# Optimization experiments

Hardware: AMD Instinct MI355X
Metric: run time of the kernel (lower is better)

Reference implementation:

```python
import jax, jax.numpy as jnp
import numpy as np

EMA_A = 0.4      # exponential moving average decay used in Hash_ExpMovAverage
WIN = 9          # window_size
LN_EPS = 1e-3    # keras LayerNormalization default epsilon


def setup_inputs() -> dict:
    key = jax.random.key(0)
    ks = jax.random.split(key, 8)
    B, N, D, H = 8, 4096, 256, 8
    w = lambda k, shape: jax.random.normal(k, shape, jnp.float32) * 0.05
    return {
        "x": jax.random.normal(ks[0], (B, N, D), jnp.float32),
        "head_kernel": w(ks[1], (D, H, D)),
        "head_bias": w(ks[2], (H, D)),
        "down_kernel": w(ks[3], (H, D, D)),
        "down_bias": w(ks[4], (D,)),
        "value_kernel": w(ks[5], (D, D)),
        "value_bias": w(ks[6], (D,)),
        "ln_gamma": jnp.ones((D,), jnp.float32),
        "ln_beta": jnp.zeros((D,), jnp.float32),
    }


def reference(x, head_kernel, head_bias, down_kernel, down_bias,
              value_kernel, value_bias, ln_gamma, ln_beta):
    B, N, D = x.shape
    half = (WIN - 1) // 2

    # Up_Projection: [B,N,D] -> [B,N,H,D], relu
    q = jax.nn.relu(jnp.einsum('bnd,dhe->bnhe', x, head_kernel) + head_bias)

    # ---- Neighborhoods_Arrangement ----
    # Neighborhood_SimHash: sign codes from relu activations, summed over heads
    codes = 2.0 * jnp.minimum(jnp.ceil(q), 1.0) - 1.0        # [B,N,H,D]
    lsh = jnp.sum(codes, axis=-2)                            # [B,N,D]
    # Hash_ExpMovAverage: sort descending along D, add positional encoding, EMA dot
    pos = jnp.argsort(-lsh, axis=-1)                         # descending order
    lsh_sorted = jnp.take_along_axis(lsh, pos, axis=-1)
    pf = pos.astype(jnp.float32)
    freq = 10.0 ** (-(pf / jnp.float32(D)))                  # 1 / 10**powers
    pe = jnp.sin(freq) * (pf % 2) + jnp.cos(freq) * (1.0 - pf % 2)
    vals = lsh_sorted + pe / EMA_A
    c = EMA_A * (1.0 - EMA_A) ** jnp.arange(D, dtype=jnp.float32)
    simv = jnp.einsum('bnd,d->bn', vals, c)                  # [B,N]
    order = jnp.argsort(simv, axis=-1)                       # ascending
    q = jnp.take_along_axis(q, order[:, :, None, None], axis=1)  # reorder tokens

    # Down_Projection: [B,N,H,D] -> [B,N,D], relu
    q = jax.nn.relu(jnp.einsum('bnhd,hde->bne', q, down_kernel) + down_bias)

    # (matches tile-first / extract_patches / tile-last concat in the original)
    starts = jnp.clip(jnp.arange(N) - half, 0, N - WIN)      # [N]
    widx = starts[:, None] + jnp.arange(WIN)[None, :]
    keyw = q[:, widx]

    scale = jnp.sqrt(jnp.float32(D))
    scores = jax.nn.softmax(jnp.einsum('bnd,bnwd->bnw', q, keyw) / scale, axis=-1)
    value = jax.nn.relu(jnp.einsum('bnwd,de->bnwe', keyw, value_kernel) + value_bias)
    attn_out = jnp.einsum('bnwd,bnw->bnd', value, scores)

    # Residual with ORIGINAL (un-permuted) inputs + LayerNorm (keras default eps)
    y = attn_out + x
    mu = jnp.mean(y, axis=-1, keepdims=True)
    var = jnp.var(y, axis=-1, keepdims=True)
    return (y - mu) / jnp.sqrt(var + LN_EPS) * ln_gamma + ln_beta
```

## Files before the change

### kernel.cpp

```cpp
#include <hip/hip_runtime.h>

constexpr int Bc = 8, Nc = 4096;

using short8 = __attribute__((ext_vector_type(8))) short;
using f32x4  = __attribute__((ext_vector_type(4))) float;

static __device__ __forceinline__ unsigned short f2bf(float f) {
    unsigned u = __float_as_uint(f);
    u += 0x7fffu + ((u >> 16) & 1u);
    return (unsigned short)(u >> 16);
}
static __device__ __forceinline__ int swz(int r, int k) {
    return (r << 9) + ((k << 1) ^ ((r & 7) << 4));
}

#define GBIN_CAP 320
#define GUARD    0.012f

__global__ __launch_bounds__(256)
void k0_wdt(const float* __restrict__ Wd, unsigned short* __restrict__ WdT)
{
    __shared__ float tile[64][65];
    const int h  = blockIdx.x >> 4;
    const int t  = blockIdx.x & 15;
    const int kb = (t >> 2) * 64, eb = (t & 3) * 64;
    const int tid = threadIdx.x;
    {
        const int krow = tid >> 2, ec = (tid & 3) * 16;
        const float* src = Wd + h * 65536 + (kb + krow) * 256 + eb + ec;
        #pragma unroll
        for (int i = 0; i < 4; ++i) {
            float4 v = *reinterpret_cast<const float4*>(src + i * 4);
            tile[krow][ec + i * 4 + 0] = v.x;
            tile[krow][ec + i * 4 + 1] = v.y;
            tile[krow][ec + i * 4 + 2] = v.z;
            tile[krow][ec + i * 4 + 3] = v.w;
        }
    }
    __syncthreads();
    {
        const int erow = tid >> 2, dc = (tid & 3) * 16;
        unsigned short o[16];
        #pragma unroll
        for (int i = 0; i < 16; ++i) o[i] = f2bf(tile[dc + i][erow]);
        unsigned short* dst = WdT + h * 65536 + (eb + erow) * 256 + kb + dc;
        *reinterpret_cast<short8*>(dst)     = *reinterpret_cast<short8*>(&o[0]);
        *reinterpret_cast<short8*>(dst + 8) = *reinterpret_cast<short8*>(&o[8]);
    }
}

__global__ __launch_bounds__(256)
void k0_wht(const float* __restrict__ Wh, unsigned short* __restrict__ WhH,
            float* __restrict__ WhT)
{
    __shared__ float tile[64][65];
    const int h  = blockIdx.x >> 4;
    const int t  = blockIdx.x & 15;
    const int kb = (t >> 2) * 64, eb = (t & 3) * 64;
    const int tid = threadIdx.x;
    {
        const int krow = tid >> 2, ec = (tid & 3) * 16;
        const float* src = Wh + (kb + krow) * 2048 + h * 256 + eb + ec;
        #pragma unroll
        for (int i = 0; i < 4; ++i) {
            float4 v = *reinterpret_cast<const float4*>(src + i * 4);
            tile[krow][ec + i * 4 + 0] = v.x;
            tile[krow][ec + i * 4 + 1] = v.y;
            tile[krow][ec + i * 4 + 2] = v.z;
            tile[krow][ec + i * 4 + 3] = v.w;
        }
    }
    __syncthreads();
    {
        const int erow = tid >> 2, dc = (tid & 3) * 16;
        unsigned short o[16];
        float of[16];
        #pragma unroll
        for (int i = 0; i < 16; ++i) {
            of[i] = tile[dc + i][erow];
            o[i] = f2bf(of[i]);
        }
        const long base = (long)h * 65536 + (eb + erow) * 256 + kb + dc;
        *reinterpret_cast<short8*>(WhH + base)     = *reinterpret_cast<short8*>(&o[0]);
        *reinterpret_cast<short8*>(WhH + base + 8) = *reinterpret_cast<short8*>(&o[8]);
        #pragma unroll
        for (int i = 0; i < 16; i += 4)
            *reinterpret_cast<float4*>(WhT + base + i) = *reinterpret_cast<const float4*>(&of[i]);
    }
}

__global__ __launch_bounds__(256)
void k0_wvt(const float* __restrict__ Wv, unsigned short* __restrict__ WvT)
{
    __shared__ float tile[64][65];
    const int t  = blockIdx.x;
    const int kb = (t >> 2) * 64, eb = (t & 3) * 64;
    const int tid = threadIdx.x;
    {
        const int krow = tid >> 2, ec = (tid & 3) * 16;
        const float* src = Wv + (kb + krow) * 256 + eb + ec;
        #pragma unroll
        for (int i = 0; i < 4; ++i) {
            float4 v = *reinterpret_cast<const float4*>(src + i * 4);
            tile[krow][ec + i * 4 + 0] = v.x;
            tile[krow][ec + i * 4 + 1] = v.y;
            tile[krow][ec + i * 4 + 2] = v.z;
            tile[krow][ec + i * 4 + 3] = v.w;
        }
    }
    __syncthreads();
    {
        const int erow = tid >> 2, dc = (tid & 3) * 16;
        unsigned short o[16];
        #pragma unroll
        for (int i = 0; i < 16; ++i) o[i] = f2bf(tile[dc + i][erow]);
        unsigned short* dst = WvT + (eb + erow) * 256 + kb + dc;
        *reinterpret_cast<short8*>(dst)     = *reinterpret_cast<short8*>(&o[0]);
        *reinterpret_cast<short8*>(dst + 8) = *reinterpret_cast<short8*>(&o[8]);
    }
}

__global__ __launch_bounds__(256, 3)
void k1a_head(const float* __restrict__ x, const float* __restrict__ bh,
              const unsigned short* __restrict__ WhH,
              unsigned short* __restrict__ q, int* __restrict__ gcnt, int* __restrict__ gls)
{
    __shared__ __align__(16) char SM[16384];

    const int tid = threadIdx.x;
    const long rowbase = (long)blockIdx.x * 32;
    const int h = blockIdx.y;
    const int wavei = tid >> 6, lane = tid & 63;
    const int mrow = lane & 15, kgrp = lane >> 4;
    const int ebase = wavei * 64 + mrow;
    const int kfo = kgrp * 8;
    const unsigned short* whh = WhH + ((long)h << 16);

    short8 hB[4][4];
    #pragma unroll
    for (int i = 0; i < 4; ++i)
        #pragma unroll
        for (int nf = 0; nf < 4; ++nf)
            hB[i][nf] = *reinterpret_cast<const short8*>(
                &whh[(ebase + nf * 16) * 256 + i * 32 + kfo]);

    {
        const int r = tid >> 3, kc = (tid & 7) * 32;
        const float* src = x + (rowbase + r) * 256 + kc;
        unsigned short oh[32];
        #pragma unroll
        for (int i = 0; i < 32; i += 4) {
            float4 v = *reinterpret_cast<const float4*>(src + i);
            oh[i + 0] = f2bf(v.x); oh[i + 1] = f2bf(v.y);
            oh[i + 2] = f2bf(v.z); oh[i + 3] = f2bf(v.w);
        }
        #pragma unroll
        for (int i = 0; i < 32; i += 8)
            *reinterpret_cast<short8*>(SM + swz(r, kc + i)) =
                *reinterpret_cast<short8*>(&oh[i]);
    }
    __syncthreads();

    f32x4 hacc[2][4];
    #pragma unroll
    for (int mt = 0; mt < 2; ++mt)
        #pragma unroll
        for (int nf = 0; nf < 4; ++nf) hacc[mt][nf] = (f32x4){0.f, 0.f, 0.f, 0.f};
    #pragma unroll
    for (int kt = 0; kt < 8; ++kt) {
        const int k0 = kt * 32 + kfo;
        short8 a0 = *reinterpret_cast<const short8*>(SM + swz(mrow, k0));
        short8 a1 = *reinterpret_cast<const short8*>(SM + swz(16 + mrow, k0));
        #pragma unroll
        for (int nf = 0; nf < 4; ++nf) {
            hacc[0][nf] = __builtin_amdgcn_mfma_f32_16x16x32_bf16(a0, hB[kt & 3][nf], hacc[0][nf], 0, 0, 0);
            hacc[1][nf] = __builtin_amdgcn_mfma_f32_16x16x32_bf16(a1, hB[kt & 3][nf], hacc[1][nf], 0, 0, 0);
        }
        if (kt < 4) {
            #pragma unroll
            for (int nf = 0; nf < 4; ++nf)
                hB[kt][nf] = *reinterpret_cast<const short8*>(
                    &whh[(ebase + nf * 16) * 256 + (kt + 4) * 32 + kfo]);
        }
    }
    float bias[4];
    #pragma unroll
    for (int nf = 0; nf < 4; ++nf) bias[nf] = bh[(h << 8) + ebase + nf * 16];
    __syncthreads();
    const int bin = (int)blockIdx.x * 8 + h;
    #pragma unroll
    for (int mt = 0; mt < 2; ++mt) {
        #pragma unroll
        for (int nf = 0; nf < 4; ++nf) {
            const int e = ebase + nf * 16;
            #pragma unroll
            for (int reg = 0; reg < 4; ++reg) {
                const int r = mt * 16 + kgrp * 4 + reg;
                const float pre = __fadd_rn(hacc[mt][nf][reg], bias[nf]);
                if (fabsf(pre) < GUARD) {
                    int idx = atomicAdd(&gcnt[bin], 1);
                    if (idx < GBIN_CAP)
                        gls[bin * GBIN_CAP + idx] =
                            r | (e << 5) | ((pre > 0.0f ? 1 : 0) << 13);
                }
                *reinterpret_cast<unsigned short*>(SM + swz(r, e)) =
                    f2bf(fmaxf(pre, 0.0f));
            }
        }
    }
    __syncthreads();
    {
        const int r = tid >> 3, ec = (tid & 7) * 32;
        unsigned short* dst = q + (rowbase + r) * 2048 + (h << 8) + ec;
        #pragma unroll
        for (int i = 0; i < 4; ++i)
            *reinterpret_cast<short8*>(dst + i * 8) =
                *reinterpret_cast<short8*>(SM + swz(r, ec + i * 8));
    }
}

__global__ __launch_bounds__(256, 3)
void k1b_down(const unsigned short* __restrict__ q,
              const unsigned short* __restrict__ WdT, const float* __restrict__ bd,
              float* __restrict__ z)
{
    __shared__ __align__(16) char SM[16384];

    const int tid = threadIdx.x;
    const long rowbase = (long)blockIdx.x * 32;
    const int wavei = tid >> 6, lane = tid & 63;
    const int mrow = lane & 15, kgrp = lane >> 4;
    const int ebase = wavei * 64 + mrow;
    const int kfo = kgrp * 8;

    short8 dB[4][4];
    #pragma unroll
    for (int i = 0; i < 4; ++i)
        #pragma unroll
        for (int nf = 0; nf < 4; ++nf)
            dB[i][nf] = *reinterpret_cast<const short8*>(
                &WdT[(ebase + nf * 16) * 256 + i * 32 + kfo]);

    f32x4 dacc[2][4];
    #pragma unroll
    for (int mt = 0; mt < 2; ++mt)
        #pragma unroll
        for (int nf = 0; nf < 4; ++nf) dacc[mt][nf] = (f32x4){0.f, 0.f, 0.f, 0.f};

    for (int kc = 0; kc < 8; ++kc) {
        const unsigned short* wdh = WdT + ((long)kc << 16);
        {
            const int r = tid >> 3, kb2 = (tid & 7) * 32;
            const unsigned short* src = q + (rowbase + r) * 2048 + (kc << 8) + kb2;
            short8 t0 = *reinterpret_cast<const short8*>(src);
            short8 t1 = *reinterpret_cast<const short8*>(src + 8);
            short8 t2 = *reinterpret_cast<const short8*>(src + 16);
            short8 t3 = *reinterpret_cast<const short8*>(src + 24);
            *reinterpret_cast<short8*>(SM + swz(r, kb2))      = t0;
            *reinterpret_cast<short8*>(SM + swz(r, kb2 + 8))  = t1;
            *reinterpret_cast<short8*>(SM + swz(r, kb2 + 16)) = t2;
            *reinterpret_cast<short8*>(SM + swz(r, kb2 + 24)) = t3;
        }
        __syncthreads();
        #pragma unroll
        for (int ks = 0; ks < 8; ++ks) {
            const int k0 = ks * 32 + kfo;
            short8 a0 = *reinterpret_cast<const short8*>(SM + swz(mrow, k0));
            short8 a1 = *reinterpret_cast<const short8*>(SM + swz(16 + mrow, k0));
            #pragma unroll
            for (int nf = 0; nf < 4; ++nf) {
                dacc[0][nf] = __builtin_amdgcn_mfma_f32_16x16x32_bf16(a0, dB[ks & 3][nf], dacc[0][nf], 0, 0, 0);
                dacc[1][nf] = __builtin_amdgcn_mfma_f32_16x16x32_bf16(a1, dB[ks & 3][nf], dacc[1][nf], 0, 0, 0);
            }
            if (ks < 4) {
                #pragma unroll
                for (int nf = 0; nf < 4; ++nf)
                    dB[ks][nf] = *reinterpret_cast<const short8*>(
                        &wdh[(ebase + nf * 16) * 256 + (ks + 4) * 32 + kfo]);
            } else if (kc < 7) {
                #pragma unroll
                for (int nf = 0; nf < 4; ++nf)
                    dB[ks - 4][nf] = *reinterpret_cast<const short8*>(
                        &WdT[((long)(kc + 1) << 16) + (ebase + nf * 16) * 256 + (ks - 4) * 32 + kfo]);
            }
        }
        __syncthreads();
    }
    #pragma unroll
    for (int mt = 0; mt < 2; ++mt) {
        #pragma unroll
        for (int nf = 0; nf < 4; ++nf) {
            const int e = ebase + nf * 16;
            const float b = bd[e];
            #pragma unroll
            for (int reg = 0; reg < 4; ++reg)
                z[(rowbase + mt * 16 + kgrp * 4 + reg) * 256 + e] =
                    fmaxf(dacc[mt][nf][reg] + b, 0.0f);
        }
    }
}

#define R_VALQ 0
#define R_LSH8 32768
#define R_PE   40960
#define R_CF   41984
#define R_CNT  43008
#define R_CCN  45056
#define R_CLS  45060
#define R_CLS_CAP 128

__global__ __launch_bounds__(256, 2)
void k1r_lsh_simv(const unsigned short* __restrict__ q, const float* __restrict__ x,
                  const float* __restrict__ WhT, const float* __restrict__ bh,
                  const int* __restrict__ gcnt, const int* __restrict__ gls,
                  float* __restrict__ simv)
{
    __shared__ __align__(16) char SM[45576];
    const int tid = threadIdx.x;
    const long rowbase = (long)blockIdx.x * 32;

    {
        const int d = tid;
        const float u = -((float)d * 0.00390625f);
        const float freq = (float)pow(10.0, (double)u);
        const float pe = (d & 1) ? (float)sin((double)freq)
                                 : (float)cos((double)freq);
        ((float*)(SM + R_PE))[d] = __fdiv_rn(pe, 0.4f);
        ((float*)(SM + R_CF))[d] = __fmul_rn(0.4f, (float)pow((double)0.6f, (double)d));
    }
    if (tid == 0) *(int*)(SM + R_CCN) = 0;
    {
        const int r = tid >> 3, ec = (tid & 7) * 32;
        int acc[32];
        #pragma unroll
        for (int j = 0; j < 32; ++j) acc[j] = 0;
        for (int h = 0; h < 8; ++h) {
            const unsigned short* src = q + (rowbase + r) * 2048 + (h << 8) + ec;
            #pragma unroll
            for (int i = 0; i < 4; ++i) {
                short8 v8 = *reinterpret_cast<const short8*>(src + i * 8);
                #pragma unroll
                for (int j = 0; j < 8; ++j)
                    acc[i * 8 + j] += ((unsigned short)v8[j] != 0) ? 1 : -1;
            }
        }
        signed char* lsh8 = (signed char*)(SM + R_LSH8);
        #pragma unroll
        for (int j = 0; j < 32; ++j)
            lsh8[(ec + j) * 32 + r] = (signed char)acc[j];
    }
    __syncthreads();
    for (int h = 0; h < 8; ++h) {
        const int bin = (int)blockIdx.x * 8 + h;
        int n = gcnt[bin];
        n = n < GBIN_CAP ? n : GBIN_CAP;
        for (int i = tid; i < n; i += 256) {
            const int ent = gls[bin * GBIN_CAP + i];
            const int r = ent & 31, e = (ent >> 5) & 255;
            const int fs = ((ent >> 13) & 1) ? 1 : -1;
            const float* xr = x + (rowbase + r) * 256;
            const float* wrow = WhT + (((long)h << 8) + e) * 256;
            float acc = 0.0f;
            for (int k = 0; k < 256; k += 4) {
                float4 xv = *reinterpret_cast<const float4*>(xr + k);
                float4 wv = *reinterpret_cast<const float4*>(wrow + k);
                acc = fmaf(xv.x, wv.x, acc);
                acc = fmaf(xv.y, wv.y, acc);
                acc = fmaf(xv.z, wv.z, acc);
                acc = fmaf(xv.w, wv.w, acc);
            }
            const float pre = __fadd_rn(acc, bh[h * 256 + e]);
            const int es = (pre > 0.0f) ? 1 : -1;
            if (es != fs) {
                int ci = atomicAdd((int*)(SM + R_CCN), 1);
                if (ci < R_CLS_CAP)
                    ((int*)(SM + R_CLS))[ci] = r | (e << 5) | ((es > 0 ? 1 : 0) << 13);
            }
        }
    }
    __syncthreads();
    if (tid == 0) {
        signed char* lsh8 = (signed char*)(SM + R_LSH8);
        int cn = *(int*)(SM + R_CCN);
        cn = cn < R_CLS_CAP ? cn : R_CLS_CAP;
        for (int i = 0; i < cn; ++i) {
            const int ent = ((int*)(SM + R_CLS))[i];
            const int r = ent & 31, e = (ent >> 5) & 255;
            const int d = ((ent >> 13) & 1) ? 2 : -2;
            lsh8[e * 32 + r] = (signed char)(lsh8[e * 32 + r] + d);
        }
    }
    __syncthreads();
    if (tid < 32) {
        const int r = tid;
        const signed char* lsh8 = (const signed char*)(SM + R_LSH8);
        const float* pe_over = (const float*)(SM + R_PE);
        const float* c_f = (const float*)(SM + R_CF);
        int* cw = (int*)(SM + R_CNT) + r * 16;
        for (int i = 0; i < 9; ++i) cw[i] = 0;
        for (int d = 0; d < 256; ++d) {
            int vv = (int)lsh8[d * 32 + r];
            cw[(vv + 8) >> 1] += 1;
        }
        int run = 0;
        for (int bin = 8; bin >= 0; --bin) { int c0 = cw[bin]; cw[bin] = run; run += c0; }
        float* valq = (float*)(SM + R_VALQ + r * 1024);
        for (int d = 0; d < 256; ++d) {
            int vv = (int)lsh8[d * 32 + r];
            int bin = (vv + 8) >> 1;
            int j = cw[bin]++;
            valq[j] = __fadd_rn((float)vv, pe_over[d]);
        }
        float L0 = 0.f, L1 = 0.f, L2 = 0.f, L3 = 0.f,
              L4 = 0.f, L5 = 0.f, L6 = 0.f, L7 = 0.f;
        for (int i = 0; i < 256; i += 8) {
            L0 = fmaf(valq[i + 0], c_f[i + 0], L0);
            L1 = fmaf(valq[i + 1], c_f[i + 1], L1);
            L2 = fmaf(valq[i + 2], c_f[i + 2], L2);
            L3 = fmaf(valq[i + 3], c_f[i + 3], L3);
            L4 = fmaf(valq[i + 4], c_f[i + 4], L4);
            L5 = fmaf(valq[i + 5], c_f[i + 5], L5);
            L6 = fmaf(valq[i + 6], c_f[i + 6], L6);
            L7 = fmaf(valq[i + 7], c_f[i + 7], L7);
        }
        const float h0 = __fadd_rn(L0, L4);
        const float h1 = __fadd_rn(L1, L5);
        const float h2 = __fadd_rn(L2, L6);
        const float h3 = __fadd_rn(L3, L7);
        simv[rowbase + r] = __fadd_rn(__fadd_rn(h0, h2), __fadd_rn(h1, h3));
    }
}

#define XSH_OFF  0
#define QTB_OFF  16384
#define LSH8_OFF 32768
#define PE_OFF   40960
#define CF_OFF   41984
#define CNT_OFF  43008
#define FCN_OFF  45056
#define CCN_OFF  45060
#define FLS_OFF  45064
#define CLS_OFF  49160
#define FLS_CAP  1024
#define CLS_CAP  96

__global__ __launch_bounds__(256, 3)
void k1_fused(const float* __restrict__ x,
              const float* __restrict__ bh,
              const float* __restrict__ WhT,
              const unsigned short* __restrict__ WhH,
              const unsigned short* __restrict__ WdT, const float* __restrict__ bd,
              float* __restrict__ z, float* __restrict__ simv)
{
    __shared__ __align__(16) char SM[49600];
    const int tid = threadIdx.x;
    const long rowbase = (long)blockIdx.x * 32;
    const int wavei = tid >> 6, lane = tid & 63;
    const int mrow = lane & 15, kgrp = lane >> 4;
    const int ebase = wavei * 64 + mrow;
    const int kfo = kgrp * 8;

    short8 hB[3][4], dB[3][4];
    #pragma unroll
    for (int i = 0; i < 2; ++i)
        #pragma unroll
        for (int nf = 0; nf < 4; ++nf)
            hB[i][nf] = *reinterpret_cast<const short8*>(
                &WhH[(ebase + nf * 16) * 256 + i * 32 + kfo]);
    {
        const int d = tid;
        const float u = -((float)d * 0.00390625f);
        const float freq = (float)pow(10.0, (double)u);
        const float pe = (d & 1) ? (float)sin((double)freq)
                                 : (float)cos((double)freq);
        ((float*)(SM + PE_OFF))[d] = __fdiv_rn(pe, 0.4f);
        ((float*)(SM + CF_OFF))[d] = __fmul_rn(0.4f, (float)pow((double)0.6f, (double)d));
    }
    if (tid == 0) { *(int*)(SM + FCN_OFF) = 0; *(int*)(SM + CCN_OFF) = 0; }
    {
        const int r = tid >> 3, kc = (tid & 7) * 32;
        const float* src = x + (rowbase + r) * 256 + kc;
        unsigned short oh[32];
        #pragma unroll
        for (int i = 0; i < 32; i += 4) {
            float4 v = *reinterpret_cast<const float4*>(src + i);
            oh[i + 0] = f2bf(v.x); oh[i + 1] = f2bf(v.y);
            oh[i + 2] = f2bf(v.z); oh[i + 3] = f2bf(v.w);
        }
        #pragma unroll
        for (int i = 0; i < 32; i += 8)
            *reinterpret_cast<short8*>(SM + XSH_OFF + swz(r, kc + i)) =
                *reinterpret_cast<short8*>(&oh[i]);
    }
    unsigned lshp[4] = {0u, 0u, 0u, 0u};
    f32x4 dacc[2][4];
    #pragma unroll
    for (int mt = 0; mt < 2; ++mt)
        #pragma unroll
        for (int nf = 0; nf < 4; ++nf) dacc[mt][nf] = (f32x4){0.f, 0.f, 0.f, 0.f};
    __syncthreads();
    for (int h = 0; h < 8; ++h) {
        const unsigned short* whh = WhH + ((long)h << 16);
        const unsigned short* wdh = WdT + ((long)h << 16);
        float bias[4];
        #pragma unroll
        for (int nf = 0; nf < 4; ++nf) bias[nf] = bh[(h << 8) + ebase + nf * 16];
        f32x4 hacc[2][4];
        #pragma unroll
        for (int mt = 0; mt < 2; ++mt)
            #pragma unroll
            for (int nf = 0; nf < 4; ++nf) hacc[mt][nf] = (f32x4){0.f, 0.f, 0.f, 0.f};
        #pragma unroll
        for (int kt = 0; kt < 8; ++kt) {
            const int k0 = kt * 32 + kfo;
            short8 a0 = *reinterpret_cast<const short8*>(SM + XSH_OFF + swz(mrow, k0));
            short8 a1 = *reinterpret_cast<const short8*>(SM + XSH_OFF + swz(16 + mrow, k0));
            if (kt < 6) {
                #pragma unroll
                for (int nf = 0; nf < 4; ++nf)
                    hB[(kt + 2) % 3][nf] = *reinterpret_cast<const short8*>(
                        &whh[(ebase + nf * 16) * 256 + (kt + 2) * 32 + kfo]);
            }
            #pragma unroll
            for (int nf = 0; nf < 4; ++nf) {
                hacc[0][nf] = __builtin_amdgcn_mfma_f32_16x16x32_bf16(a0, hB[kt % 3][nf], hacc[0][nf], 0, 0, 0);
                hacc[1][nf] = __builtin_amdgcn_mfma_f32_16x16x32_bf16(a1, hB[kt % 3][nf], hacc[1][nf], 0, 0, 0);
            }
        }
        #pragma unroll
        for (int i = 0; i < 2; ++i)
            #pragma unroll
            for (int nf = 0; nf < 4; ++nf)
                dB[i][nf] = *reinterpret_cast<const short8*>(
                    &wdh[(ebase + nf * 16) * 256 + i * 32 + kfo]);
        #pragma unroll
        for (int mt = 0; mt < 2; ++mt) {
            #pragma unroll
            for (int nf = 0; nf < 4; ++nf) {
                const int e = ebase + nf * 16;
                #pragma unroll
                for (int reg = 0; reg < 4; ++reg) {
                    const int r = mt * 16 + kgrp * 4 + reg;
                    const float pre = __fadd_rn(hacc[mt][nf][reg], bias[nf]);
                    const unsigned pos = (pre > 0.0f) ? 1u : 0u;
                    const int j = mt * 16 + nf * 4 + reg;
                    lshp[j >> 3] += pos << (4 * (j & 7));
                    if (fabsf(pre) < GUARD) {
                        int idx = atomicAdd((int*)(SM + FCN_OFF), 1);
                        if (idx < FLS_CAP)
                            ((int*)(SM + FLS_OFF))[idx] =
                                r | (e << 5) | (h << 13) | ((int)pos << 16);
                    }
                    *reinterpret_cast<unsigned short*>(SM + QTB_OFF + swz(r, e)) =
                        f2bf(fmaxf(pre, 0.0f));
                }
            }
        }
        __syncthreads();
        #pragma unroll
        for (int ks = 0; ks < 8; ++ks) {
            const int k0 = ks * 32 + kfo;
            short8 a0 = *reinterpret_cast<const short8*>(SM + QTB_OFF + swz(mrow, k0));
            short8 a1 = *reinterpret_cast<const short8*>(SM + QTB_OFF + swz(16 + mrow, k0));
            if (ks < 6) {
                #pragma unroll
                for (int nf = 0; nf < 4; ++nf)
                    dB[(ks + 2) % 3][nf] = *reinterpret_cast<const short8*>(
                        &wdh[(ebase + nf * 16) * 256 + (ks + 2) * 32 + kfo]);
            } else if (h < 7) {
                const int i = ks - 6;
                #pragma unroll
                for (int nf = 0; nf < 4; ++nf)
                    hB[i][nf] = *reinterpret_cast<const short8*>(
                        &WhH[((long)(h + 1) << 16) + (ebase + nf * 16) * 256 + i * 32 + kfo]);
            }
            #pragma unroll
            for (int nf = 0; nf < 4; ++nf) {
                dacc[0][nf] = __builtin_amdgcn_mfma_f32_16x16x32_bf16(a0, dB[ks % 3][nf], dacc[0][nf], 0, 0, 0);
                dacc[1][nf] = __builtin_amdgcn_mfma_f32_16x16x32_bf16(a1, dB[ks % 3][nf], dacc[1][nf], 0, 0, 0);
            }
        }
        __syncthreads();
    }
    #pragma unroll
    for (int mt = 0; mt < 2; ++mt) {
        #pragma unroll
        for (int nf = 0; nf < 4; ++nf) {
            const int e = ebase + nf * 16;
            const float b = bd[e];
            #pragma unroll
            for (int reg = 0; reg < 4; ++reg)
                z[(rowbase + mt * 16 + kgrp * 4 + reg) * 256 + e] =
                    fmaxf(dacc[mt][nf][reg] + b, 0.0f);
        }
    }
    {
        signed char* lsh8 = (signed char*)(SM + LSH8_OFF);
        #pragma unroll
        for (int mt = 0; mt < 2; ++mt)
            #pragma unroll
            for (int nf = 0; nf < 4; ++nf) {
                const int e = ebase + nf * 16;
                #pragma unroll
                for (int reg = 0; reg < 4; ++reg) {
                    const int r = mt * 16 + kgrp * 4 + reg;
                    const int j = mt * 16 + nf * 4 + reg;
                    const unsigned p = (lshp[j >> 3] >> (4 * (j & 7))) & 15u;
                    lsh8[e * 32 + r] = (signed char)(2 * (int)p - 8);
                }
            }
    }
    __syncthreads();
    {
        int n = *((int*)(SM + FCN_OFF));
        n = n < FLS_CAP ? n : FLS_CAP;
        for (int i = tid; i < n; i += 256) {
            const int ent = ((int*)(SM + FLS_OFF))[i];
            const int r = ent & 31, e = (ent >> 5) & 255, hh2 = (ent >> 13) & 7;
            const int fs = ((ent >> 16) & 1) ? 1 : -1;
            const float* xr = x + (rowbase + r) * 256;
            const float* wrow = WhT + (((long)hh2 << 8) + e) * 256;
            float acc = 0.0f;
            for (int k = 0; k < 256; k += 4) {
                float4 xv = *reinterpret_cast<const float4*>(xr + k);
                float4 wv = *reinterpret_cast<const float4*>(wrow + k);
                acc = fmaf(xv.x, wv.x, acc);
                acc = fmaf(xv.y, wv.y, acc);
                acc = fmaf(xv.z, wv.z, acc);
                acc = fmaf(xv.w, wv.w, acc);
            }
            const float pre = __fadd_rn(acc, bh[hh2 * 256 + e]);
            const int es = (pre > 0.0f) ? 1 : -1;
            if (es != fs) {
                int ci = atomicAdd((int*)(SM + CCN_OFF), 1);
                if (ci < CLS_CAP)
                    ((int*)(SM + CLS_OFF))[ci] = r | (e << 5) | ((es > 0 ? 1 : 0) << 13);
            }
        }
    }
    __syncthreads();
    if (tid == 0) {
        signed char* lsh8 = (signed char*)(SM + LSH8_OFF);
        int cn = *((int*)(SM + CCN_OFF));
        cn = cn < CLS_CAP ? cn : CLS_CAP;
        for (int i = 0; i < cn; ++i) {
            const int ent = ((int*)(SM + CLS_OFF))[i];
            const int r = ent & 31, e = (ent >> 5) & 255;
            const int d = ((ent >> 13) & 1) ? 2 : -2;
            lsh8[e * 32 + r] = (signed char)(lsh8[e * 32 + r] + d);
        }
    }
    __syncthreads();
    if (tid < 32) {
        const int r = tid;
        const signed char* lsh8 = (const signed char*)(SM + LSH8_OFF);
        const float* pe_over = (const float*)(SM + PE_OFF);
        const float* c_f = (const float*)(SM + CF_OFF);
        int* cw = (int*)(SM + CNT_OFF) + r * 16;
        for (int i = 0; i < 9; ++i) cw[i] = 0;
        for (int d = 0; d < 256; ++d) {
            int vv = (int)lsh8[d * 32 + r];
            cw[(vv + 8) >> 1] += 1;
        }
        int run = 0;
        for (int bin = 8; bin >= 0; --bin) { int c0 = cw[bin]; cw[bin] = run; run += c0; }
        float* valq = (float*)(SM + r * 1024);
        for (int d = 0; d < 256; ++d) {
            int vv = (int)lsh8[d * 32 + r];
            int bin = (vv + 8) >> 1;
            int j = cw[bin]++;
            valq[j] = __fadd_rn((float)vv, pe_over[d]);
        }
        float L0 = 0.f, L1 = 0.f, L2 = 0.f, L3 = 0.f,
              L4 = 0.f, L5 = 0.f, L6 = 0.f, L7 = 0.f;
        for (int i = 0; i < 256; i += 8) {
            L0 = fmaf(valq[i + 0], c_f[i + 0], L0);
            L1 = fmaf(valq[i + 1], c_f[i + 1], L1);
            L2 = fmaf(valq[i + 2], c_f[i + 2], L2);
            L3 = fmaf(valq[i + 3], c_f[i + 3], L3);
            L4 = fmaf(valq[i + 4], c_f[i + 4], L4);
            L5 = fmaf(valq[i + 5], c_f[i + 5], L5);
            L6 = fmaf(valq[i + 6], c_f[i + 6], L6);
            L7 = fmaf(valq[i + 7], c_f[i + 7], L7);
        }
        const float h0 = __fadd_rn(L0, L4);
        const float h1 = __fadd_rn(L1, L5);
        const float h2 = __fadd_rn(L2, L6);
        const float h3 = __fadd_rn(L3, L7);
        simv[rowbase + r] = __fadd_rn(__fadd_rn(h0, h2), __fadd_rn(h1, h3));
    }
}

__global__ __launch_bounds__(256)
void k2_rank(const float* __restrict__ simv, int* __restrict__ order)
{
    __shared__ float s_l[4096];
    const int b = blockIdx.x >> 4;
    const int chunk = blockIdx.x & 15;
    const float* S = simv + (long)b * 4096;
    for (int i = threadIdx.x; i < 4096; i += 256) s_l[i] = S[i];
    __syncthreads();
    const int n = chunk * 256 + threadIdx.x;
    const float key = s_l[n];
    int cnt = 0;
    for (int m = 0; m < 4096; ++m) {
        float sm = s_l[m];
        cnt += (sm < key) ? 1 : ((sm == key && m < n) ? 1 : 0);
    }
    order[(long)b * 4096 + cnt] = n;
}

__global__ __launch_bounds__(256, 3)
void k3_value(const float* __restrict__ z, const int* __restrict__ order,
              const unsigned short* __restrict__ WvT, const float* __restrict__ bv,
              float* __restrict__ v)
{
    __shared__ __align__(16) unsigned short ZB[32 * 256];
    __shared__ int ord[32];
    const int tid = threadIdx.x;
    const long rowbase = (long)blockIdx.x * 32;
    const long bbase = (rowbase >> 12) << 12;
    const int wavei = tid >> 6, lane = tid & 63;
    const int mrow = lane & 15, kgrp = lane >> 4;
    const int ebase = wavei * 64 + mrow;
    const int kfo = kgrp * 8;

    if (tid < 32) ord[tid] = order[rowbase + tid];

    short8 vB[3][4];
    #pragma unroll
    for (int i = 0; i < 2; ++i)
        #pragma unroll
        for (int nf = 0; nf < 4; ++nf)
            vB[i][nf] = *reinterpret_cast<const short8*>(
                &WvT[(ebase + nf * 16) * 256 + i * 32 + kfo]);

    __syncthreads();
    {
        const int r = tid >> 3, kc = (tid & 7) * 32;
        const float* src = z + (bbase + ord[r]) * 256 + kc;
        unsigned short oh[32];
        #pragma unroll
        for (int i = 0; i < 32; i += 4) {
            float4 vv = *reinterpret_cast<const float4*>(src + i);
            oh[i + 0] = f2bf(vv.x); oh[i + 1] = f2bf(vv.y);
            oh[i + 2] = f2bf(vv.z); oh[i + 3] = f2bf(vv.w);
        }
        #pragma unroll
        for (int i = 0; i < 32; i += 8)
            *reinterpret_cast<short8*>((char*)ZB + swz(r, kc + i)) =
                *reinterpret_cast<short8*>(&oh[i]);
    }
    __syncthreads();

    f32x4 acc[2][4];
    #pragma unroll
    for (int mt = 0; mt < 2; ++mt)
        #pragma unroll
        for (int nf = 0; nf < 4; ++nf) acc[mt][nf] = (f32x4){0.f, 0.f, 0.f, 0.f};
    #pragma unroll
    for (int kt = 0; kt < 8; ++kt) {
        const int k0 = kt * 32 + kfo;
        short8 a0 = *reinterpret_cast<const short8*>((char*)ZB + swz(mrow, k0));
        short8 a1 = *reinterpret_cast<const short8*>((char*)ZB + swz(16 + mrow, k0));
        if (kt < 6) {
            #pragma unroll
            for (int nf = 0; nf < 4; ++nf)
                vB[(kt + 2) % 3][nf] = *reinterpret_cast<const short8*>(
                    &WvT[(ebase + nf * 16) * 256 + (kt + 2) * 32 + kfo]);
        }
        #pragma unroll
        for (int nf = 0; nf < 4; ++nf) {
            acc[0][nf] = __builtin_amdgcn_mfma_f32_16x16x32_bf16(a0, vB[kt % 3][nf], acc[0][nf], 0, 0, 0);
            acc[1][nf] = __builtin_amdgcn_mfma_f32_16x16x32_bf16(a1, vB[kt % 3][nf], acc[1][nf], 0, 0, 0);
        }
    }
    #pragma unroll
    for (int mt = 0; mt < 2; ++mt) {
        #pragma unroll
        for (int nf = 0; nf < 4; ++nf) {
            const int e = ebase + nf * 16;
            const float b = bv[e];
            #pragma unroll
            for (int reg = 0; reg < 4; ++reg)
                v[(rowbase + mt * 16 + kgrp * 4 + reg) * 256 + e] =
                    fmaxf(acc[mt][nf][reg] + b, 0.0f);
        }
    }
}

__global__ __launch_bounds__(256)
void k4_attn_ln(const float* __restrict__ z, const float* __restrict__ v,
                const int* __restrict__ order, const float* __restrict__ x,
                const float* __restrict__ gamma, const float* __restrict__ beta,
                float* __restrict__ out)
{
    const int tid = threadIdx.x;
    const int wv = tid >> 6, lane = tid & 63;
    const long row = (long)blockIdx.x * 4 + wv;
    const int n = (int)(row & 4095);
    const long bbase = row - n;
    int start = n - 4;
    start = start < 0 ? 0 : start;
    start = start > (Nc - 9) ? (Nc - 9) : start;
    const int d0 = lane * 4;

    const int srcq = order[bbase + n];
    float4 q4 = *reinterpret_cast<const float4*>(&z[(bbase + srcq) * 256 + d0]);

    float t[9];
    #pragma unroll
    for (int w = 0; w < 9; ++w) {
        int srcm = order[bbase + start + w];
        float4 kv = *reinterpret_cast<const float4*>(&z[(bbase + srcm) * 256 + d0]);
        float p = q4.x * kv.x + q4.y * kv.y + q4.z * kv.z + q4.w * kv.w;
        #pragma unroll
        for (int off = 32; off > 0; off >>= 1) p += __shfl_xor(p, off);
        t[w] = p * 0.0625f;
    }
    float mx = t[0];
    #pragma unroll
    for (int w = 1; w < 9; ++w) mx = fmaxf(mx, t[w]);
    float pw[9], psum = 0.0f;
    #pragma unroll
    for (int w = 0; w < 9; ++w) { pw[w] = expf(t[w] - mx); psum += pw[w]; }
    const float pinv = 1.0f / psum;

    float4 a = make_float4(0.f, 0.f, 0.f, 0.f);
    #pragma unroll
    for (int w = 0; w < 9; ++w) {
        float4 vv = *reinterpret_cast<const float4*>(&v[(bbase + start + w) * 256 + d0]);
        float s = pw[w] * pinv;
        a.x = fmaf(vv.x, s, a.x);
        a.y = fmaf(vv.y, s, a.y);
        a.z = fmaf(vv.z, s, a.z);
        a.w = fmaf(vv.w, s, a.w);
    }
    float4 xv = *reinterpret_cast<const float4*>(&x[(bbase + n) * 256 + d0]);
    float4 y = make_float4(a.x + xv.x, a.y + xv.y, a.z + xv.z, a.w + xv.w);

    float s1 = y.x + y.y + y.z + y.w;
    float s2 = y.x * y.x + y.y * y.y + y.z * y.z + y.w * y.w;
    #pragma unroll
    for (int off = 32; off > 0; off >>= 1) {
        s1 += __shfl_xor(s1, off);
        s2 += __shfl_xor(s2, off);
    }
    const float mu = s1 * (1.0f / 256.0f);
    const float var = s2 * (1.0f / 256.0f) - mu * mu;
    const float istd = 1.0f / sqrtf(var + 0.001f);

    float4 g4 = *reinterpret_cast<const float4*>(&gamma[d0]);
    float4 b4 = *reinterpret_cast<const float4*>(&beta[d0]);
    float4 o;
    o.x = (y.x - mu) * istd * g4.x + b4.x;
    o.y = (y.y - mu) * istd * g4.y + b4.y;
    o.z = (y.z - mu) * istd * g4.z + b4.z;
    o.w = (y.w - mu) * istd * g4.w + b4.w;
    *reinterpret_cast<float4*>(&out[row * 256 + d0]) = o;
}

extern "C" void kernel_launch(void* const* d_in, const int* in_sizes, int n_in,
                              void* d_out, int out_size, void* d_ws, size_t ws_size,
                              hipStream_t stream)
{
    const float* x  = (const float*)d_in[0];
    const float* Wh = (const float*)d_in[1];
    const float* bh = (const float*)d_in[2];
    const float* Wd = (const float*)d_in[3];
    const float* bd = (const float*)d_in[4];
    const float* Wv = (const float*)d_in[5];
    const float* bv = (const float*)d_in[6];
    const float* g  = (const float*)d_in[7];
    const float* be = (const float*)d_in[8];
    float* out = (float*)d_out;

    char* ws = (char*)d_ws;
    float*          z     = (float*)ws;
    float*          v     = (float*)(ws + 33554432);
    float*          simv  = (float*)(ws + 67108864);
    int*            order = (int*)(ws + 67239936);
    unsigned short* WdT   = (unsigned short*)(ws + 67371008);
    unsigned short* WhH   = (unsigned short*)(ws + 68419584);
    float*          WhT   = (float*)(ws + 69468160);
    unsigned short* WvT   = (unsigned short*)(ws + 71565312);
    unsigned short* q     = (unsigned short*)(ws + 71696384);
    int*            gcnt  = (int*)(ws + 205914112);
    int*            gls   = (int*)(ws + 205946880);

    const bool big = ws_size >= 216432640ULL;
    const int rows = Bc * Nc;

    k0_wdt<<<dim3(128), dim3(256), 0, stream>>>(Wd, WdT);
    k0_wht<<<dim3(128), dim3(256), 0, stream>>>(Wh, WhH, WhT);
    k0_wvt<<<dim3(16), dim3(256), 0, stream>>>(Wv, WvT);
    if (big) {
        hipMemsetAsync(gcnt, 0, 32768, stream);
        k1a_head<<<dim3(1024, 8), dim3(256), 0, stream>>>(x, bh, WhH, q, gcnt, gls);
        k1b_down<<<dim3(1024), dim3(256), 0, stream>>>(q, WdT, bd, z);
        k1r_lsh_simv<<<dim3(1024), dim3(256), 0, stream>>>(q, x, WhT, bh, gcnt, gls, simv);
    } else {
        k1_fused<<<dim3(rows / 32), dim3(256), 0, stream>>>(x, bh, WhT, WhH, WdT, bd, z, simv);
    }
    k2_rank<<<dim3(Bc * 16), dim3(256), 0, stream>>>(simv, order);
    k3_value<<<dim3(rows / 32), dim3(256), 0, stream>>>(z, order, WvT, bv, v);
    k4_attn_ln<<<dim3(rows / 4), dim3(256), 0, stream>>>(z, v, order, x, g, be, out);
}
```

Before: 817.9 us.

## Fuse LSH/simv computation into down-projection kernel to reuse loaded q tiles

The separate k1r_lsh_simv kernel is merged into k1b_down. While the down-projection staging loop loads bf16 q tiles, the new code also counts nonzero signs per head in packed 4-bit counters, which removes the second full read of q (about 134 MB) and one kernel launch. Shared memory grows from 16 KB to about 45 KB and the kernel keeps launch_bounds(256,3), so occupancy may drop. The serial tail (guard corrections, sort, EMA) now runs after the MFMA work inside the same block.

```diff
diff --git a/kernel.cpp b/kernel.cpp
--- a/kernel.cpp
+++ b/kernel.cpp
@@ -219,12 +219,24 @@
     }
 }
 
+#define B_VALQ 0
+#define B_LSH8 32768
+#define B_PE   40960
+#define B_CF   41984
+#define B_CNT  43008
+#define B_CCN  45056
+#define B_CLS  45060
+#define B_CLS_CAP 128
+
 __global__ __launch_bounds__(256, 3)
 void k1b_down(const unsigned short* __restrict__ q,
               const unsigned short* __restrict__ WdT, const float* __restrict__ bd,
-              float* __restrict__ z)
-{
-    __shared__ __align__(16) char SM[16384];
+              const float* __restrict__ x, const float* __restrict__ WhT,
+              const float* __restrict__ bh,
+              const int* __restrict__ gcnt, const int* __restrict__ gls,
+              float* __restrict__ z, float* __restrict__ simv)
+{
+    __shared__ __align__(16) char SM[45576];
 
     const int tid = threadIdx.x;
     const long rowbase = (long)blockIdx.x * 32;
@@ -241,11 +253,24 @@
             dB[i][nf] = *reinterpret_cast<const short8*>(
                 &WdT[(ebase + nf * 16) * 256 + i * 32 + kfo]);
 
+    {
+        const int d = tid;
+        const float u = -((float)d * 0.00390625f);
+        const float freq = (float)pow(10.0, (double)u);
+        const float pe = (d & 1) ? (float)sin((double)freq)
+                                 : (float)cos((double)freq);
+        ((float*)(SM + B_PE))[d] = __fdiv_rn(pe, 0.4f);
+        ((float*)(SM + B_CF))[d] = __fmul_rn(0.4f, (float)pow((double)0.6f, (double)d));
+    }
+    if (tid == 0) *(int*)(SM + B_CCN) = 0;
+
     f32x4 dacc[2][4];
     #pragma unroll
     for (int mt = 0; mt < 2; ++mt)
         #pragma unroll
         for (int nf = 0; nf < 4; ++nf) dacc[mt][nf] = (f32x4){0.f, 0.f, 0.f, 0.f};
+    unsigned lshp[4] = {0u, 0u, 0u, 0u};
+    __syncthreads();
 
     for (int kc = 0; kc < 8; ++kc) {
         const unsigned short* wdh = WdT + ((long)kc << 16);
@@ -260,6 +285,13 @@
             *reinterpret_cast<short8*>(SM + swz(r, kb2 + 8))  = t1;
             *reinterpret_cast<short8*>(SM + swz(r, kb2 + 16)) = t2;
             *reinterpret_cast<short8*>(SM + swz(r, kb2 + 24)) = t3;
+            #pragma unroll
+            for (int j = 0; j < 8; ++j) {
+                lshp[0] += (((unsigned short)t0[j] != 0) ? 1u : 0u) << (4 * (j & 7));
+                lshp[1] += (((unsigned short)t1[j] != 0) ? 1u : 0u) << (4 * (j & 7));
+                lshp[2] += (((unsigned short)t2[j] != 0) ? 1u : 0u) << (4 * (j & 7));
+                lshp[3] += (((unsigned short)t3[j] != 0) ? 1u : 0u) << (4 * (j & 7));
+            }
         }
         __syncthreads();
         #pragma unroll
@@ -298,56 +330,16 @@
                     fmaxf(dacc[mt][nf][reg] + b, 0.0f);
         }
     }
-}
-
-#define R_VALQ 0
-#define R_LSH8 32768
-#define R_PE   40960
-#define R_CF   41984
-#define R_CNT  43008
-#define R_CCN  45056
-#define R_CLS  45060
-#define R_CLS_CAP 128
-
-__global__ __launch_bounds__(256, 2)
-void k1r_lsh_simv(const unsigned short* __restrict__ q, const float* __restrict__ x,
-                  const float* __restrict__ WhT, const float* __restrict__ bh,
-                  const int* __restrict__ gcnt, const int* __restrict__ gls,
-                  float* __restrict__ simv)
-{
-    __shared__ __align__(16) char SM[45576];
-    const int tid = threadIdx.x;
-    const long rowbase = (long)blockIdx.x * 32;
-
-    {
-        const int d = tid;
-        const float u = -((float)d * 0.00390625f);
-        const float freq = (float)pow(10.0, (double)u);
-        const float pe = (d & 1) ? (float)sin((double)freq)
-                                 : (float)cos((double)freq);
-        ((float*)(SM + R_PE))[d] = __fdiv_rn(pe, 0.4f);
-        ((float*)(SM + R_CF))[d] = __fmul_rn(0.4f, (float)pow((double)0.6f, (double)d));
-    }
-    if (tid == 0) *(int*)(SM + R_CCN) = 0;
-    {
-        const int r = tid >> 3, ec = (tid & 7) * 32;
-        int acc[32];
-        #pragma unroll
-        for (int j = 0; j < 32; ++j) acc[j] = 0;
-        for (int h = 0; h < 8; ++h) {
-            const unsigned short* src = q + (rowbase + r) * 2048 + (h << 8) + ec;
-            #pragma unroll
-            for (int i = 0; i < 4; ++i) {
-                short8 v8 = *reinterpret_cast<const short8*>(src + i * 8);
-                #pragma unroll
-                for (int j = 0; j < 8; ++j)
-                    acc[i * 8 + j] += ((unsigned short)v8[j] != 0) ? 1 : -1;
-            }
-        }
-        signed char* lsh8 = (signed char*)(SM + R_LSH8);
-        #pragma unroll
-        for (int j = 0; j < 32; ++j)
-            lsh8[(ec + j) * 32 + r] = (signed char)acc[j];
+    {
+        signed char* lsh8 = (signed char*)(SM + B_LSH8);
+        const int r = tid >> 3, e0 = (tid & 7) * 32;
+        #pragma unroll
+        for (int i = 0; i < 4; ++i)
+            #pragma unroll
+            for (int j = 0; j < 8; ++j) {
+                const unsigned p = (lshp[i] >> (4 * j)) & 15u;
+                lsh8[(e0 + i * 8 + j) * 32 + r] = (signed char)(2 * (int)p - 8);
+            }
     }
     __syncthreads();
     for (int h = 0; h < 8; ++h) {
@@ -372,19 +364,19 @@
             const float pre = __fadd_rn(acc, bh[h * 256 + e]);
             const int es = (pre > 0.0f) ? 1 : -1;
             if (es != fs) {
-                int ci = atomicAdd((int*)(SM + R_CCN), 1);
-                if (ci < R_CLS_CAP)
-                    ((int*)(SM + R_CLS))[ci] = r | (e << 5) | ((es > 0 ? 1 : 0) << 13);
+                int ci = atomicAdd((int*)(SM + B_CCN), 1);
+                if (ci < B_CLS_CAP)
+                    ((int*)(SM + B_CLS))[ci] = r | (e << 5) | ((es > 0 ? 1 : 0) << 13);
             }
         }
     }
     __syncthreads();
     if (tid == 0) {
-        signed char* lsh8 = (signed char*)(SM + R_LSH8);
-        int cn = *(int*)(SM + R_CCN);
-        cn = cn < R_CLS_CAP ? cn : R_CLS_CAP;
+        signed char* lsh8 = (signed char*)(SM + B_LSH8);
+        int cn = *(int*)(SM + B_CCN);
+        cn = cn < B_CLS_CAP ? cn : B_CLS_CAP;
         for (int i = 0; i < cn; ++i) {
-            const int ent = ((int*)(SM + R_CLS))[i];
+            const int ent = ((int*)(SM + B_CLS))[i];
             const int r = ent & 31, e = (ent >> 5) & 255;
             const int d = ((ent >> 13) & 1) ? 2 : -2;
             lsh8[e * 32 + r] = (signed char)(lsh8[e * 32 + r] + d);
@@ -393,10 +385,10 @@
     __syncthreads();
     if (tid < 32) {
         const int r = tid;
-        const signed char* lsh8 = (const signed char*)(SM + R_LSH8);
-        const float* pe_over = (const float*)(SM + R_PE);
-        const float* c_f = (const float*)(SM + R_CF);
-        int* cw = (int*)(SM + R_CNT) + r * 16;
+        const signed char* lsh8 = (const signed char*)(SM + B_LSH8);
+        const float* pe_over = (const float*)(SM + B_PE);
+        const float* c_f = (const float*)(SM + B_CF);
+        int* cw = (int*)(SM + B_CNT) + r * 16;
         for (int i = 0; i < 9; ++i) cw[i] = 0;
         for (int d = 0; d < 256; ++d) {
             int vv = (int)lsh8[d * 32 + r];
@@ -404,7 +396,7 @@
         }
         int run = 0;
         for (int bin = 8; bin >= 0; --bin) { int c0 = cw[bin]; cw[bin] = run; run += c0; }
-        float* valq = (float*)(SM + R_VALQ + r * 1024);
+        float* valq = (float*)(SM + B_VALQ + r * 1024);
         for (int d = 0; d < 256; ++d) {
             int vv = (int)lsh8[d * 32 + r];
             int bin = (vv + 8) >> 1;
@@ -897,8 +889,7 @@
     if (big) {
         hipMemsetAsync(gcnt, 0, 32768, stream);
         k1a_head<<<dim3(1024, 8), dim3(256), 0, stream>>>(x, bh, WhH, q, gcnt, gls);
-        k1b_down<<<dim3(1024), dim3(256), 0, stream>>>(q, WdT, bd, z);
-        k1r_lsh_simv<<<dim3(1024), dim3(256), 0, stream>>>(q, x, WhT, bh, gcnt, gls, simv);
+        k1b_down<<<dim3(1024), dim3(256), 0, stream>>>(q, WdT, bd, x, WhT, bh, gcnt, gls, z, simv);
     } else {
         k1_fused<<<dim3(rows / 32), dim3(256), 0, stream>>>(x, bh, WhT, WhH, WdT, bd, z, simv);
     }
```

After: 771.6 us. 5.7% less time.
